# Kernel tuning notes

Hardware: AMD Instinct MI355X
Metric: run time of the kernel (lower is better)

The kernel has to match this reference:

```python
import jax, jax.numpy as jnp
import numpy as np

ALPHA = 3          # init: alpha
EPS = 1e-6         # init: eps
LOSS_WEIGHT = 1.0  # init: loss_weight
N = 500000


def box2corners(box):
    # (n,5) (x,y,w,h,a) -> (n,4,2) corners, standard differentiable rotated-IoU layout
    x, y, w, h, a = (box[:, i] for i in range(5))
    dx = jnp.array([0.5, -0.5, -0.5, 0.5], box.dtype) * w[:, None]
    dy = jnp.array([0.5, 0.5, -0.5, -0.5], box.dtype) * h[:, None]
    c = jnp.cos(a)[:, None]
    s = jnp.sin(a)[:, None]
    return jnp.stack([dx * c - dy * s + x[:, None], dx * s + dy * c + y[:, None]], -1)


def cross2(a, b):
    return a[..., 0] * b[..., 1] - a[..., 1] * b[..., 0]


def box_intersection(c1, c2):
    # all 4x4 edge-pair segment intersections -> (n,16,2) points, (n,16) validity mask
    p1 = c1[:, :, None, :]                              # (n,4,1,2)
    d1 = jnp.roll(c1, -1, 1)[:, :, None, :] - p1
    q1 = c2[:, None, :, :]                              # (n,1,4,2)
    d2 = jnp.roll(c2, -1, 1)[:, None, :, :] - q1
    den = cross2(d1, d2)
    den_safe = jnp.where(jnp.abs(den) < 1e-12, 1e-12, den)
    t = cross2(q1 - p1, d2) / den_safe
    u = cross2(q1 - p1, d1) / den_safe
    mask = (t > 0) & (t < 1) & (u > 0) & (u < 1)
    pts = (p1 + t[..., None] * d1) * mask[..., None]    # zero invalid, as in torch ref
    n = c1.shape[0]
    return pts.reshape(n, 16, 2), mask.reshape(n, 16)


def corners_in_box(pts, corners):
    # which of pts (n,4,2) lie inside the rotated box given by corners (n,4,2)
    a = corners[:, 0:1]
    b = corners[:, 1:2]
    d = corners[:, 3:4]
    ab = b - a
    ad = d - a
    am = pts - a
    r_ab = jnp.sum(ab * am, -1) / jnp.maximum(jnp.sum(ab * ab, -1), 1e-12)
    r_ad = jnp.sum(ad * am, -1) / jnp.maximum(jnp.sum(ad * ad, -1), 1e-12)
    tol = 1e-6
    return (r_ab > -tol) & (r_ab < 1 + tol) & (r_ad > -tol) & (r_ad < 1 + tol)


def sorted_polygon_area(verts, mask):
    # verts (n,24,2), mask (n,24): sort valid vertices by angle around centroid, shoelace
    mf = mask[..., None].astype(verts.dtype)
    cnt = jnp.maximum(jnp.sum(mf, axis=1, keepdims=True), 1.0)
    center = jnp.sum(verts * mf, axis=1, keepdims=True) / cnt
    rel = verts - center
    ang = jnp.where(mask, jnp.arctan2(rel[..., 1], rel[..., 0]), 1e6)  # invalid -> last
    order = jnp.argsort(ang, axis=1)
    v = jnp.take_along_axis(verts, order[..., None], axis=1)
    ms = jnp.take_along_axis(mask, order, axis=1)
    v = jnp.where(ms[..., None], v, v[:, 0:1, :])  # pad invalid slots with first valid vtx
    nxt = jnp.roll(v, -1, axis=1)
    return 0.5 * jnp.abs(jnp.sum(cross2(v, nxt), axis=1))


def enclosing_smallest(c1, c2):
    # smallest enclosing rotated rectangle over the 8 corners (rotating-calipers over edges)
    pts = jnp.concatenate([c1, c2], axis=1)  # (n,8,2)
    edges = jnp.concatenate([jnp.roll(c1, -1, 1) - c1, jnp.roll(c2, -1, 1) - c2], axis=1)
    u = edges / jnp.maximum(jnp.linalg.norm(edges, axis=-1, keepdims=True), 1e-12)
    perp = jnp.stack([-u[..., 1], u[..., 0]], -1)
    px = jnp.einsum('npc,ndc->npd', pts, u)      # (n,8pts,8dirs)
    py = jnp.einsum('npc,ndc->npd', pts, perp)
    w = px.max(1) - px.min(1)
    h = py.max(1) - py.min(1)
    idx = jnp.argmin(w * h, axis=1)[:, None]
    return jnp.take_along_axis(w, idx, 1)[:, 0], jnp.take_along_axis(h, idx, 1)[:, 0]


def _giou_loss(pred, target):
    c1 = box2corners(pred)
    c2 = box2corners(target)
    inter_pts, inter_mask = box_intersection(c1, c2)
    m1 = corners_in_box(c1, c2)
    m2 = corners_in_box(c2, c1)
    verts = jnp.concatenate([c1, c2, inter_pts], axis=1)  # (n,24,2)
    mask = jnp.concatenate([m1, m2, inter_mask], axis=1)  # (n,24)
    inter_area = sorted_polygon_area(verts, mask)
    union = pred[:, 2] * pred[:, 3] + target[:, 2] * target[:, 3] - inter_area
    ious = jnp.maximum(inter_area / union, EPS)  # ious.clamp(min=eps)
    w, h = enclosing_smallest(c1, c2)
    area_c = w * h
    giou = ious ** ALPHA - ((area_c - union) / area_c) ** ALPHA
    loss = 1.0 - giou
    return LOSS_WEIGHT * jnp.mean(loss)  # reduction='mean'


def setup_inputs() -> dict:
    key = jax.random.key(0)
    ks = jax.random.split(key, 6)
    xy = jax.random.uniform(ks[0], (N, 2), minval=0.0, maxval=1024.0)
    wh1 = jax.random.uniform(ks[1], (N, 2), minval=8.0, maxval=128.0)
    a1 = jax.random.uniform(ks[2], (N, 1), minval=-1.5, maxval=1.5)
    pred = jnp.concatenate([xy, wh1, a1], axis=1)
    xy2 = xy + jax.random.normal(ks[3], (N, 2)) * 8.0  # jitter so boxes mostly overlap
    wh2 = jax.random.uniform(ks[4], (N, 2), minval=8.0, maxval=128.0)
    a2 = jax.random.uniform(ks[5], (N, 1), minval=-1.5, maxval=1.5)
    target = jnp.concatenate([xy2, wh2, a2], axis=1)
    return {"pred": pred, "target": target}


def reference(pred, target):
    return _giou_loss(pred, target)
```

## Files before the change

### kernel.cpp

```cpp
#include <hip/hip_runtime.h>

__device__ __forceinline__ float frcp(float x){ return __builtin_amdgcn_rcpf(x); }

__device__ __forceinline__ float lb_edge(float x0, float y0, float x1, float y1,
                                         float lx, float hx, float ly, float hy)
{
    float dx = x1 - x0, dy = y1 - y0;
    float idx = frcp(dx), idy = frcp(dy);
    float ta = (lx - x0) * idx, tb = (hx - x0) * idx;
    float tc = (ly - y0) * idy, td = (hy - y0) * idy;
    float tx0 = fminf(ta, tb), tx1 = fmaxf(ta, tb);
    float ty0 = fminf(tc, td), ty1 = fmaxf(tc, td);
    float t0 = fmaxf(fmaxf(tx0, ty0), 0.f);
    float t1 = fminf(fminf(tx1, ty1), 1.f);
    bool valid = t1 > t0;
    float pax = fmaf(t0, dx, x0), pay = fmaf(t0, dy, y0);
    float pbx = fmaf(t1, dx, x0), pby = fmaf(t1, dy, y0);
    float c = fmaf(pax, pby, -pay * pbx);
    return valid ? c : 0.f;
}

__device__ __forceinline__ float clip_quad(float cbx, float cby,
                                           float ux, float uy, float vx, float vy,
                                           float lx, float hx, float ly, float hy)
{
    float upx = ux + vx, upy = uy + vy;
    float umx = ux - vx, umy = uy - vy;
    float gx0 = cbx + upx, gy0 = cby + upy;
    float gx1 = cbx - umx, gy1 = cby - umy;
    float gx2 = cbx - upx, gy2 = cby - upy;
    float gx3 = cbx + umx, gy3 = cby + umy;
    float s = lb_edge(gx0, gy0, gx1, gy1, lx, hx, ly, hy);
    s += lb_edge(gx1, gy1, gx2, gy2, lx, hx, ly, hy);
    s += lb_edge(gx2, gy2, gx3, gy3, lx, hx, ly, hy);
    s += lb_edge(gx3, gy3, gx0, gy0, lx, hx, ly, hy);
    return s;
}

__global__ __launch_bounds__(256) void giou_partial_kernel(
    const float* __restrict__ pred, const float* __restrict__ target,
    float* __restrict__ partial, int n)
{
    int i = blockIdx.x * blockDim.x + threadIdx.x;
    float loss = 0.0f;
    if (i < n) {
        const float p0 = pred[5*i+0], p1 = pred[5*i+1], p2 = pred[5*i+2], p3 = pred[5*i+3], p4 = pred[5*i+4];
        const float q0 = target[5*i+0], q1 = target[5*i+1], q2 = target[5*i+2], q3 = target[5*i+3], q4 = target[5*i+4];

        const float oaX = 0.5f*(p0 - q0), oaY = 0.5f*(p1 - q1);
        const float hw1 = 0.5f*p2, hh1 = 0.5f*p3, hw2 = 0.5f*q2, hh2 = 0.5f*q3;

        const float cs1 = __cosf(p4), sn1 = __sinf(p4);
        const float cs2 = __cosf(q4), sn2 = __sinf(q4);
        const float cD = cs1*cs2 + sn1*sn2;
        const float sD = sn2*cs1 - cs2*sn1;

        const float caX =  oaX*cs1 + oaY*sn1;
        const float caY = -oaX*sn1 + oaY*cs1;
        float twoA = clip_quad(-caX, -caY,
                               cD*hw2,  sD*hw2, -sD*hh2, cD*hh2,
                               caX - hw1, caX + hw1, caY - hh1, caY + hh1);

        const float caX2 =  oaX*cs2 + oaY*sn2;
        const float caY2 = -oaX*sn2 + oaY*cs2;
        twoA += clip_quad(caX2, caY2,
                          cD*hw1, -sD*hw1, sD*hh1, cD*hh1,
                          -caX2 - hw2, -caX2 + hw2, -caY2 - hh2, -caY2 + hh2);

        float inter_area = 0.5f * fabsf(twoA);

        float unionv = p2*p3 + q2*q3 - inter_area;
        float iou = fmaxf(inter_area * frcp(unionv), 1e-6f);

        float acd = fabsf(cD), asd = fabsf(sD);
        float eBx = hw2*acd + hh2*asd, eBy = hw2*asd + hh2*acd;
        float w1 = fmaxf(caX + hw1, -caX + eBx) - fminf(caX - hw1, -caX - eBx);
        float h1 = fmaxf(caY + hh1, -caY + eBy) - fminf(caY - hh1, -caY - eBy);
        float a1 = w1*h1;
        float eAx = hw1*acd + hh1*asd, eAy = hw1*asd + hh1*acd;
        float w2 = fmaxf(caX2 + eAx, -caX2 + hw2) - fminf(caX2 - eAx, -caX2 - hw2);
        float h2 = fmaxf(caY2 + eAy, -caY2 + hh2) - fminf(caY2 - eAy, -caY2 - hh2);
        float a2 = w2*h2;

        float area_c = (a2 < a1) ? a2 : a1;

        float r = (area_c - unionv) * frcp(area_c);
        float giou = iou*iou*iou - r*r*r;
        loss = 1.0f - giou;
    }

    #pragma unroll
    for (int off = 32; off; off >>= 1) loss += __shfl_down(loss, off, 64);
    __shared__ float smem[4];
    int lane = threadIdx.x & 63, wid = threadIdx.x >> 6;
    if (lane == 0) smem[wid] = loss;
    __syncthreads();
    if (threadIdx.x == 0) {
        partial[blockIdx.x] = smem[0] + smem[1] + smem[2] + smem[3];
    }
}

__global__ __launch_bounds__(256) void reduce_final_kernel(
    const float* __restrict__ partial, int nb, float* __restrict__ out, float invn)
{
    float s = 0.f;
    for (int i = threadIdx.x; i < nb; i += 256) s += partial[i];
    #pragma unroll
    for (int off = 32; off; off >>= 1) s += __shfl_down(s, off, 64);
    __shared__ float smem[4];
    int lane = threadIdx.x & 63, wid = threadIdx.x >> 6;
    if (lane == 0) smem[wid] = s;
    __syncthreads();
    if (threadIdx.x == 0) {
        out[0] = (smem[0] + smem[1] + smem[2] + smem[3]) * invn;
    }
}

extern "C" void kernel_launch(void* const* d_in, const int* in_sizes, int n_in,
                              void* d_out, int out_size, void* d_ws, size_t ws_size,
                              hipStream_t stream) {
    const float* pred   = (const float*)d_in[0];
    const float* target = (const float*)d_in[1];
    float* out = (float*)d_out;
    float* partial = (float*)d_ws;
    int n  = in_sizes[0] / 5;
    int nb = (n + 255) / 256;
    giou_partial_kernel<<<nb, 256, 0, stream>>>(pred, target, partial, n);
    reduce_final_kernel<<<1, 256, 0, stream>>>(partial, nb, out, 1.0f/(float)n);
}
```

Measured before the change: 15.51 us.

## Fuse final reduction via packed fixed-point atomic counter and vectorize clipping math

Replaces the second reduction kernel with a single 64-bit atomic that packs a block-completion count in the high 16 bits and a fixed-point partial sum in the low 48 bits, so the last block writes the mean directly. This removes a kernel launch and the pass over the partials buffer, at the cost of a memset and fixed-point rounding of each block sum. The Liang-Barsky clipping is also rewritten with float2 vectors and precomputed edge reciprocals shared between opposite edges, reducing the number of rcp instructions. The fixed-point encoding assumes block sums are non-negative and that the count fits in 16 bits; nb is about 1954 here, so it does.

```diff
diff --git a/kernel.cpp b/kernel.cpp
--- a/kernel.cpp
+++ b/kernel.cpp
@@ -1,45 +1,43 @@
 #include <hip/hip_runtime.h>
 
+typedef float v2 __attribute__((ext_vector_type(2)));
+
 __device__ __forceinline__ float frcp(float x){ return __builtin_amdgcn_rcpf(x); }
+__device__ __forceinline__ v2 rcp2(v2 a){ v2 r; r.x = frcp(a.x); r.y = frcp(a.y); return r; }
+__device__ __forceinline__ v2 min2(v2 a, v2 b){ v2 r; r.x = fminf(a.x,b.x); r.y = fminf(a.y,b.y); return r; }
+__device__ __forceinline__ v2 max2(v2 a, v2 b){ v2 r; r.x = fmaxf(a.x,b.x); r.y = fmaxf(a.y,b.y); return r; }
 
-__device__ __forceinline__ float lb_edge(float x0, float y0, float x1, float y1,
-                                         float lx, float hx, float ly, float hy)
+__device__ __forceinline__ float lb_edge(v2 p0, v2 d, v2 id, v2 lo, v2 hi)
 {
-    float dx = x1 - x0, dy = y1 - y0;
-    float idx = frcp(dx), idy = frcp(dy);
-    float ta = (lx - x0) * idx, tb = (hx - x0) * idx;
-    float tc = (ly - y0) * idy, td = (hy - y0) * idy;
-    float tx0 = fminf(ta, tb), tx1 = fmaxf(ta, tb);
-    float ty0 = fminf(tc, td), ty1 = fmaxf(tc, td);
-    float t0 = fmaxf(fmaxf(tx0, ty0), 0.f);
-    float t1 = fminf(fminf(tx1, ty1), 1.f);
-    bool valid = t1 > t0;
-    float pax = fmaf(t0, dx, x0), pay = fmaf(t0, dy, y0);
-    float pbx = fmaf(t1, dx, x0), pby = fmaf(t1, dy, y0);
-    float c = fmaf(pax, pby, -pay * pbx);
-    return valid ? c : 0.f;
+    v2 ta = (lo - p0) * id;
+    v2 tb = (hi - p0) * id;
+    v2 tmn = min2(ta, tb);
+    v2 tmx = max2(ta, tb);
+    float t0 = fmaxf(fmaxf(tmn.x, tmn.y), 0.f);
+    float t1 = fminf(fminf(tmx.x, tmx.y), 1.f);
+    v2 pa = (v2){t0, t0} * d + p0;
+    v2 pb = (v2){t1, t1} * d + p0;
+    float c = fmaf(pa.x, pb.y, -(pa.y * pb.x));
+    return (t1 > t0) ? c : 0.f;
 }
 
-__device__ __forceinline__ float clip_quad(float cbx, float cby,
-                                           float ux, float uy, float vx, float vy,
-                                           float lx, float hx, float ly, float hy)
+__device__ __forceinline__ float clip_quad(v2 cb, v2 u, v2 v, v2 lo, v2 hi)
 {
-    float upx = ux + vx, upy = uy + vy;
-    float umx = ux - vx, umy = uy - vy;
-    float gx0 = cbx + upx, gy0 = cby + upy;
-    float gx1 = cbx - umx, gy1 = cby - umy;
-    float gx2 = cbx - upx, gy2 = cby - upy;
-    float gx3 = cbx + umx, gy3 = cby + umy;
-    float s = lb_edge(gx0, gy0, gx1, gy1, lx, hx, ly, hy);
-    s += lb_edge(gx1, gy1, gx2, gy2, lx, hx, ly, hy);
-    s += lb_edge(gx2, gy2, gx3, gy3, lx, hx, ly, hy);
-    s += lb_edge(gx3, gy3, gx0, gy0, lx, hx, ly, hy);
+    v2 up = u + v, um = u - v;
+    v2 g0 = cb + up, g1 = cb - um, g2 = cb - up, g3 = cb + um;
+    v2 du2 = u + u, dv2 = v + v;
+    v2 idu = rcp2(du2), idv = rcp2(dv2);
+    float s = lb_edge(g0, -du2, -idu, lo, hi);
+    s += lb_edge(g1, -dv2, -idv, lo, hi);
+    s += lb_edge(g2,  du2,  idu, lo, hi);
+    s += lb_edge(g3,  dv2,  idv, lo, hi);
     return s;
 }
 
-__global__ __launch_bounds__(256) void giou_partial_kernel(
+__global__ __launch_bounds__(256) void giou_kernel(
     const float* __restrict__ pred, const float* __restrict__ target,
-    float* __restrict__ partial, int n)
+    unsigned long long* __restrict__ counter, float* __restrict__ out,
+    int n, int nb, double dscale)
 {
     int i = blockIdx.x * blockDim.x + threadIdx.x;
     float loss = 0.0f;
@@ -47,25 +45,25 @@
         const float p0 = pred[5*i+0], p1 = pred[5*i+1], p2 = pred[5*i+2], p3 = pred[5*i+3], p4 = pred[5*i+4];
         const float q0 = target[5*i+0], q1 = target[5*i+1], q2 = target[5*i+2], q3 = target[5*i+3], q4 = target[5*i+4];
 
-        const float oaX = 0.5f*(p0 - q0), oaY = 0.5f*(p1 - q1);
         const float hw1 = 0.5f*p2, hh1 = 0.5f*p3, hw2 = 0.5f*q2, hh2 = 0.5f*q3;
+        const v2 oa = { 0.5f*(p0 - q0), 0.5f*(p1 - q1) };
 
         const float cs1 = __cosf(p4), sn1 = __sinf(p4);
         const float cs2 = __cosf(q4), sn2 = __sinf(q4);
         const float cD = cs1*cs2 + sn1*sn2;
         const float sD = sn2*cs1 - cs2*sn1;
 
-        const float caX =  oaX*cs1 + oaY*sn1;
-        const float caY = -oaX*sn1 + oaY*cs1;
-        float twoA = clip_quad(-caX, -caY,
-                               cD*hw2,  sD*hw2, -sD*hh2, cD*hh2,
-                               caX - hw1, caX + hw1, caY - hh1, caY + hh1);
+        const v2 caA = oa.x * (v2){cs1, -sn1} + oa.y * (v2){sn1, cs1};
+        const v2 hA  = {hw1, hh1};
+        float twoA = clip_quad(-caA,
+                               hw2 * (v2){cD, sD}, hh2 * (v2){-sD, cD},
+                               caA - hA, caA + hA);
 
-        const float caX2 =  oaX*cs2 + oaY*sn2;
-        const float caY2 = -oaX*sn2 + oaY*cs2;
-        twoA += clip_quad(caX2, caY2,
-                          cD*hw1, -sD*hw1, sD*hh1, cD*hh1,
-                          -caX2 - hw2, -caX2 + hw2, -caY2 - hh2, -caY2 + hh2);
+        const v2 caB = oa.x * (v2){cs2, -sn2} + oa.y * (v2){sn2, cs2};
+        const v2 hB  = {hw2, hh2};
+        twoA += clip_quad(caB,
+                          hw1 * (v2){cD, -sD}, hh1 * (v2){sD, cD},
+                          -caB - hB, -caB + hB);
 
         float inter_area = 0.5f * fabsf(twoA);
 
@@ -74,12 +72,12 @@
 
         float acd = fabsf(cD), asd = fabsf(sD);
         float eBx = hw2*acd + hh2*asd, eBy = hw2*asd + hh2*acd;
-        float w1 = fmaxf(caX + hw1, -caX + eBx) - fminf(caX - hw1, -caX - eBx);
-        float h1 = fmaxf(caY + hh1, -caY + eBy) - fminf(caY - hh1, -caY - eBy);
+        float w1 = fmaxf(caA.x + hw1, -caA.x + eBx) - fminf(caA.x - hw1, -caA.x - eBx);
+        float h1 = fmaxf(caA.y + hh1, -caA.y + eBy) - fminf(caA.y - hh1, -caA.y - eBy);
         float a1 = w1*h1;
         float eAx = hw1*acd + hh1*asd, eAy = hw1*asd + hh1*acd;
-        float w2 = fmaxf(caX2 + eAx, -caX2 + hw2) - fminf(caX2 - eAx, -caX2 - hw2);
-        float h2 = fmaxf(caY2 + eAy, -caY2 + hh2) - fminf(caY2 - eAy, -caY2 - hh2);
+        float w2 = fmaxf(caB.x + eAx, -caB.x + hw2) - fminf(caB.x - eAx, -caB.x - hw2);
+        float h2 = fmaxf(caB.y + eAy, -caB.y + hh2) - fminf(caB.y - eAy, -caB.y - hh2);
         float a2 = w2*h2;
 
         float area_c = (a2 < a1) ? a2 : a1;
@@ -95,24 +93,16 @@
     int lane = threadIdx.x & 63, wid = threadIdx.x >> 6;
     if (lane == 0) smem[wid] = loss;
     __syncthreads();
+
     if (threadIdx.x == 0) {
-        partial[blockIdx.x] = smem[0] + smem[1] + smem[2] + smem[3];
-    }
-}
-
-__global__ __launch_bounds__(256) void reduce_final_kernel(
-    const float* __restrict__ partial, int nb, float* __restrict__ out, float invn)
-{
-    float s = 0.f;
-    for (int i = threadIdx.x; i < nb; i += 256) s += partial[i];
-    #pragma unroll
-    for (int off = 32; off; off >>= 1) s += __shfl_down(s, off, 64);
-    __shared__ float smem[4];
-    int lane = threadIdx.x & 63, wid = threadIdx.x >> 6;
-    if (lane == 0) smem[wid] = s;
-    __syncthreads();
-    if (threadIdx.x == 0) {
-        out[0] = (smem[0] + smem[1] + smem[2] + smem[3]) * invn;
+        float bsum = smem[0] + smem[1] + smem[2] + smem[3];
+        unsigned long long fixed = (unsigned long long)llrint((double)bsum * 16777216.0);
+        unsigned long long packed = (1ULL << 48) | fixed;
+        unsigned long long old = atomicAdd(counter, packed);
+        if ((old >> 48) == (unsigned long long)(nb - 1)) {
+            unsigned long long total = (old + packed) & ((1ULL << 48) - 1ULL);
+            out[0] = (float)((double)total * dscale);
+        }
     }
 }
 
@@ -122,9 +112,10 @@
     const float* pred   = (const float*)d_in[0];
     const float* target = (const float*)d_in[1];
     float* out = (float*)d_out;
-    float* partial = (float*)d_ws;
+    unsigned long long* counter = (unsigned long long*)d_ws;
     int n  = in_sizes[0] / 5;
     int nb = (n + 255) / 256;
-    giou_partial_kernel<<<nb, 256, 0, stream>>>(pred, target, partial, n);
-    reduce_final_kernel<<<1, 256, 0, stream>>>(partial, nb, out, 1.0f/(float)n);
+    double dscale = 1.0 / (16777216.0 * (double)n);
+    hipMemsetAsync(counter, 0, 8, stream);
+    giou_kernel<<<nb, 256, 0, stream>>>(pred, target, counter, out, n, nb, dscale);
 }
```

Measured after the change: 35.69 us. +130.1%, slower.
